# Performance work log

Measured on AMD Instinct MI355X. Metric: run time of the kernel, lower is better.

## Reference

```python
import jax, jax.numpy as jnp
import numpy as np

D, H1, O, E = 1024, 4096, 1024, 8
B = 8192


def setup_inputs() -> dict:
    key = jax.random.key(0)
    k1, k2, k3, k4 = jax.random.split(key, 4)
    # kaiming_uniform_ with nonlinearity='relu': bound = sqrt(6 / fan_in), fan_in = last dim
    b_w1 = float(np.sqrt(6.0 / D))
    b_w2 = float(np.sqrt(6.0 / H1))
    x = jax.random.normal(k1, (B, D), dtype=jnp.float32)
    eid = jax.random.randint(k2, (B,), 0, E, dtype=jnp.int32)
    W1 = jax.random.uniform(k3, (E, H1, D), dtype=jnp.float32, minval=-b_w1, maxval=b_w1)
    W2 = jax.random.uniform(k4, (E, O, H1), dtype=jnp.float32, minval=-b_w2, maxval=b_w2)
    b2 = jnp.zeros((E, O), dtype=jnp.float32)
    return {"x": x, "eid": eid, "W1": W1, "W2": W2, "b2": b2}


def reference(x, eid, W1, W2, b2):
    # Per-token expert MLP: y_i = gelu(x_i @ W1[eid_i].T) @ W2[eid_i].T + b2[eid_i]
    # Dense-dispatch formulation: loop over the (small, static) expert axis,
    # compute each expert MLP on all tokens, and select per-token via mask.
    # Math is identical to the sort/gather/scatter original.
    y = jnp.zeros((x.shape[0], W2.shape[1]), dtype=x.dtype)
    for e in range(W1.shape[0]):
        h = jax.nn.gelu(x @ W1[e].T, approximate=False)   # [B, H1]
        y_e = h @ W2[e].T + b2[e]                          # [B, O]
        mask = (eid == e)[:, None].astype(x.dtype)
        y = y + mask * y_e
    return y
```

## Files before the change

### kernel.cpp

```cpp
#include <hip/hip_runtime.h>
#include <hip/hip_bf16.h>
#include <math.h>

constexpr int kD  = 1024;
constexpr int kH1 = 4096;
constexpr int kO  = 1024;
constexpr int kE  = 8;
constexpr int kB  = 8192;

constexpr int BM   = 128;
constexpr int MAXT = kB / BM + kE;

typedef __attribute__((ext_vector_type(8))) short short8;
typedef __attribute__((ext_vector_type(4))) float f32x4;

__device__ __forceinline__ unsigned short f2bf(float f) {
  unsigned int u = __float_as_uint(f);
  u += 0x7fffu + ((u >> 16) & 1u);
  return (unsigned short)(u >> 16);
}

__device__ __forceinline__ float gelu_fast(float x) {
  float u = 0.7978845608028654f * (x + 0.044715f * x * x * x);
  float eu = __expf(2.0f * u);
  float th = 1.0f - 2.0f / (eu + 1.0f);
  return 0.5f * x * (1.0f + th);
}

__device__ __forceinline__ void cvt8(const float* __restrict__ src,
                                     unsigned short* __restrict__ dst) {
  const float4* s = (const float4*)src;
  float4 f0 = s[0], f1 = s[1];
  short8 v;
  v[0] = (short)f2bf(f0.x); v[1] = (short)f2bf(f0.y);
  v[2] = (short)f2bf(f0.z); v[3] = (short)f2bf(f0.w);
  v[4] = (short)f2bf(f1.x); v[5] = (short)f2bf(f1.y);
  v[6] = (short)f2bf(f1.z); v[7] = (short)f2bf(f1.w);
  *(short8*)dst = v;
}

__global__ __launch_bounds__(256) void setup_kernel(const int* __restrict__ eid,
                                                    int* __restrict__ perm,
                                                    int* __restrict__ tiles) {
  __shared__ int cnt[kE];
  __shared__ int off[kE];
  __shared__ int cur[kE];
  int t = threadIdx.x;
  if (t < kE) { cnt[t] = 0; cur[t] = 0; }
  __syncthreads();
  for (int i = t; i < kB; i += 256) atomicAdd(&cnt[eid[i]], 1);
  __syncthreads();
  if (t == 0) {
    int o = 0, nt = 0;
    for (int e = 0; e < kE; ++e) {
      off[e] = o;
      int c = cnt[e];
      for (int r = 0; r < c; r += BM) {
        tiles[nt * 4 + 0] = e;
        tiles[nt * 4 + 1] = o + r;
        tiles[nt * 4 + 2] = (c - r < BM) ? (c - r) : BM;
        tiles[nt * 4 + 3] = 0;
        ++nt;
      }
      o += c;
    }
    for (; nt < MAXT; ++nt) {
      tiles[nt * 4 + 0] = 0; tiles[nt * 4 + 1] = 0;
      tiles[nt * 4 + 2] = 0; tiles[nt * 4 + 3] = 0;
    }
  }
  __syncthreads();
  for (int i = t; i < kB; i += 256) {
    int e = eid[i];
    int p = off[e] + atomicAdd(&cur[e], 1);
    perm[p] = i;
  }
}

constexpr int kGB = kB * kD / 8 / 256;
constexpr int kCN = kE * kH1 * kD / 8;

__global__ __launch_bounds__(256) void prep_kernel(
    const float* __restrict__ x, const int* __restrict__ perm,
    unsigned short* __restrict__ xg,
    const float* __restrict__ W1, unsigned short* __restrict__ W1b) {
  const int b = blockIdx.x;
  if (b < kGB) {
    int idx = b * 256 + threadIdx.x;
    int pos = idx >> 7;
    int c   = (idx & 127) << 3;
    cvt8(x + (size_t)perm[pos] * kD + c, xg + (size_t)pos * kD + c);
  } else {
    const int cb = b - kGB;
    const int stride = 2048 * 256;
    for (int i = cb * 256 + threadIdx.x; i < kCN; i += stride)
      cvt8(W1 + (size_t)i * 8, W1b + (size_t)i * 8);
  }
}

__global__ __launch_bounds__(256) void convert_kernel(const float* __restrict__ src,
                                                      unsigned short* __restrict__ dst,
                                                      int n8) {
  int stride = gridDim.x * 256;
  for (int i = blockIdx.x * 256 + threadIdx.x; i < n8; i += stride)
    cvt8(src + (size_t)i * 8, dst + (size_t)i * 8);
}

template <int KTOT, int N, int NPAN, int MODE, int CONVW2>
__global__ __launch_bounds__(512, 2) void gemm32_kernel(
    const unsigned short* __restrict__ Amat,
    const unsigned short* __restrict__ Bmat,
    const float* __restrict__ bias,
    const int* __restrict__ tiles,
    const int* __restrict__ perm,
    unsigned short* __restrict__ out_bf,
    float* __restrict__ out_f,
    const float* __restrict__ csrc,
    unsigned short* __restrict__ cdst) {
  extern __shared__ char lds[];
  constexpr int NKt = KTOT / 32;
  constexpr int TOTAL = MAXT * NPAN;
  constexpr int cpx = TOTAL / 8;
  constexpr int nchN = (NPAN >= 4) ? NPAN / 4 : 1;

  int bid = blockIdx.x;
  const int t = threadIdx.x;

  if constexpr (CONVW2 > 0) {
    if (bid < 256) {
      constexpr int per = kCN / 256;
      size_t u0 = (size_t)bid * per;
      for (int i = t; i < per; i += 512)
        cvt8(csrc + (u0 + i) * 8, cdst + (u0 + i) * 8);
      return;
    }
    bid -= 256;
  }

  const int id = (bid & 7) * cpx + (bid >> 3);
  const int chunk = id >> 4, a16 = id & 15;
  const int ti = (chunk / nchN) * 4 + (a16 & 3);
  const int n0 = ((chunk % nchN) * 4 + (a16 >> 2)) * 256;

  const int e  = tiles[ti * 4 + 0];
  const int rs = tiles[ti * 4 + 1];
  const int nr = tiles[ti * 4 + 2];
  if (nr == 0) return;

  const int l = t & 63;
  const int w = t >> 6;
  const int lr = l & 15, g = l >> 4;
  const int wr = w >> 2;
  const int wc = w & 3;

  const unsigned short* Bp = Bmat + (size_t)e * N * KTOT;

  const int sR = t >> 2;
  const int sG = (t & 3) ^ ((sR >> 1) & 3);
  const unsigned short* ArowS = Amat + (size_t)(rs + sR) * KTOT + sG * 8;
  const unsigned short* BrowS0 = Bp + (size_t)(n0 + sR) * KTOT + sG * 8;
  const unsigned short* BrowS1 = Bp + (size_t)(n0 + 128 + sR) * KTOT + sG * 8;

  auto stageA = [&](char* buf, int k0) {
    __builtin_amdgcn_global_load_lds(
        (const __attribute__((address_space(1))) unsigned int*)(ArowS + k0),
        (__attribute__((address_space(3))) unsigned int*)(buf + t * 16), 16, 0, 0);
  };
  auto stageB = [&](char* buf, int k0, int i) {
    const unsigned short* src = (i ? BrowS1 : BrowS0) + k0;
    __builtin_amdgcn_global_load_lds(
        (const __attribute__((address_space(1))) unsigned int*)src,
        (__attribute__((address_space(3))) unsigned int*)(buf + 8192 + i * 8192 + t * 16),
        16, 0, 0);
  };

  const int rA = wr * 64 + lr;
  const int rB = wc * 64 + lr;
  const int offA0 = rA * 64 + ((g ^ ((rA >> 1) & 3)) * 16);
  const int offB0 = 8192 + rB * 64 + ((g ^ ((rB >> 1) & 3)) * 16);

  short8 aF[4], bF[4];
  f32x4 acc[4][4] = {};

  auto readA = [&](char* buf) {
#pragma unroll
    for (int mr = 0; mr < 4; ++mr)
      aF[mr] = *(const short8*)(buf + offA0 + mr * 1024);
  };
  auto readB2 = [&](char* buf, int nclo) {
#pragma unroll
    for (int j = 0; j < 2; ++j)
      bF[nclo + j] = *(const short8*)(buf + offB0 + (nclo + j) * 1024);
  };
  auto mfmaH = [&](int nclo) {
    __builtin_amdgcn_s_setprio(1);
#pragma unroll
    for (int j = 0; j < 2; ++j)
#pragma unroll
      for (int mr = 0; mr < 4; ++mr)
        acc[nclo + j][mr] = __builtin_amdgcn_mfma_f32_16x16x32_bf16(
            aF[mr], bF[nclo + j], acc[nclo + j][mr], 0, 0, 0);
    __builtin_amdgcn_s_setprio(0);
  };

  char* b0 = lds;
  char* b1 = lds + 24576;
  char* b2 = lds + 49152;

  stageA(b0, 0);  stageB(b0, 0, 0);  stageB(b0, 0, 1);
  stageA(b1, 32); stageB(b1, 32, 0); stageB(b1, 32, 1);

#pragma unroll 1
  for (int kt = 0; kt < NKt; ++kt) {
    const int k0n = (kt + 2) * 32;
    const bool more = (kt + 2 < NKt);
    if (kt == NKt - 1) asm volatile("s_waitcnt vmcnt(0)" ::: "memory");
    else               asm volatile("s_waitcnt vmcnt(3)" ::: "memory");
    __builtin_amdgcn_s_barrier();
    readA(b0);
    readB2(b0, 0);
    if (more) stageA(b2, k0n);
    __builtin_amdgcn_s_barrier();
    mfmaH(0);
    __builtin_amdgcn_s_barrier();
    readB2(b0, 2);
    if (more) { stageB(b2, k0n, 0); stageB(b2, k0n, 1); }
    __builtin_amdgcn_s_barrier();
    mfmaH(2);
    char* tmp = b0; b0 = b1; b1 = b2; b2 = tmp;
  }

  const int lr4 = g * 4;
#pragma unroll
  for (int mr = 0; mr < 4; ++mr)
#pragma unroll
    for (int rg = 0; rg < 4; ++rg) {
      int row = wr * 64 + mr * 16 + lr4 + rg;
      if (row < nr) {
        if constexpr (MODE == 0) {
          unsigned short* dst = out_bf + (size_t)(rs + row) * N + n0 + wc * 64;
#pragma unroll
          for (int nc = 0; nc < 4; ++nc)
            dst[nc * 16 + lr] = f2bf(gelu_fast(acc[nc][mr][rg]));
        } else {
          int orig = perm[rs + row];
          float* dst = out_f + (size_t)orig * N + n0 + wc * 64;
          const float* bp = bias + (size_t)e * N + n0 + wc * 64;
#pragma unroll
          for (int nc = 0; nc < 4; ++nc)
            dst[nc * 16 + lr] = acc[nc][mr][rg] + bp[nc * 16 + lr];
        }
      }
    }
}

extern "C" void kernel_launch(void* const* d_in, const int* in_sizes, int n_in,
                              void* d_out, int out_size, void* d_ws, size_t ws_size,
                              hipStream_t stream) {
  const float* x  = (const float*)d_in[0];
  const int*  eid = (const int*)d_in[1];
  const float* W1 = (const float*)d_in[2];
  const float* W2 = (const float*)d_in[3];
  const float* b2 = (const float*)d_in[4];
  float* y = (float*)d_out;

  char* ws = (char*)d_ws;
  int* perm  = (int*)ws;
  int* tiles = (int*)(ws + 32768);
  unsigned short* xg = (unsigned short*)(ws + 36864);
  size_t xg_bytes = (size_t)(kB + 128) * kD * 2;
  unsigned short* h  = (unsigned short*)(ws + 36864 + xg_bytes);
  size_t h_bytes = (size_t)(kB + 128) * kH1 * 2;
  size_t w1b_off = 36864 + xg_bytes + h_bytes;
  unsigned short* W1b = (unsigned short*)(ws + w1b_off);
  size_t w2b_off = w1b_off + 67108864;
  const bool twobuf = ws_size >= w2b_off + 67108864;
  unsigned short* W2b = twobuf ? (unsigned short*)(ws + w2b_off) : W1b;

  auto g1f = gemm32_kernel<kD, kH1, 16, 0, 1>;
  auto g1s = gemm32_kernel<kD, kH1, 16, 0, 0>;
  auto g2  = gemm32_kernel<kH1, kO, 4, 1, 0>;
  hipFuncSetAttribute((const void*)g1f, hipFuncAttributeMaxDynamicSharedMemorySize, 73728);
  hipFuncSetAttribute((const void*)g1s, hipFuncAttributeMaxDynamicSharedMemorySize, 73728);
  hipFuncSetAttribute((const void*)g2,  hipFuncAttributeMaxDynamicSharedMemorySize, 73728);

  setup_kernel<<<1, 256, 0, stream>>>(eid, perm, tiles);

  prep_kernel<<<kGB + 2048, 256, 0, stream>>>(x, perm, xg, W1, W1b);

  if (twobuf) {
    g1f<<<256 + MAXT * 16, 512, 73728, stream>>>(
        xg, W1b, nullptr, tiles, perm, h, nullptr, W2, W2b);
  } else {
    g1s<<<MAXT * 16, 512, 73728, stream>>>(
        xg, W1b, nullptr, tiles, perm, h, nullptr, nullptr, nullptr);
    convert_kernel<<<2048, 256, 0, stream>>>(W2, W2b, kCN);
  }

  g2<<<MAXT * 4, 512, 73728, stream>>>(
      h, W2b, b2, tiles, perm, nullptr, y, nullptr, nullptr);
}
```

Before: 303.2 us.

## Split-K the second expert GEMM in two halves with a bf16 partial and a reduce pass

The second GEMM's K dimension (4096) is split into two halves, so the grid doubles from MAXT*4 to MAXT*8 blocks and the device is better filled. The first half writes fp32 results straight to y. The second half writes a bf16 partial into the reused xg buffer. A new reduce kernel adds that partial plus the bias into y. This trades an extra kernel launch, extra memory traffic and bf16 rounding of half the partial sum for more parallelism in a GEMM that previously had too few blocks.

```diff
diff --git a/kernel.cpp b/kernel.cpp
--- a/kernel.cpp
+++ b/kernel.cpp
@@ -18,6 +18,9 @@
   unsigned int u = __float_as_uint(f);
   u += 0x7fffu + ((u >> 16) & 1u);
   return (unsigned short)(u >> 16);
+}
+__device__ __forceinline__ float bf2f(unsigned short u) {
+  return __uint_as_float(((unsigned int)u) << 16);
 }
 
 __device__ __forceinline__ float gelu_fast(float x) {
@@ -118,7 +121,7 @@
     const float* __restrict__ csrc,
     unsigned short* __restrict__ cdst) {
   extern __shared__ char lds[];
-  constexpr int NKt = KTOT / 32;
+  constexpr int NKt = (MODE == 1) ? (KTOT / 64) : (KTOT / 32);
   constexpr int TOTAL = MAXT * NPAN;
   constexpr int cpx = TOTAL / 8;
   constexpr int nchN = (NPAN >= 4) ? NPAN / 4 : 1;
@@ -140,7 +143,14 @@
   const int id = (bid & 7) * cpx + (bid >> 3);
   const int chunk = id >> 4, a16 = id & 15;
   const int ti = (chunk / nchN) * 4 + (a16 & 3);
-  const int n0 = ((chunk % nchN) * 4 + (a16 >> 2)) * 256;
+  const int pancol = (chunk % nchN) * 4 + (a16 >> 2);
+
+  int n0, kb, half;
+  if constexpr (MODE == 0) {
+    n0 = pancol * 256; kb = 0; half = 0;
+  } else {
+    half = pancol >> 2; n0 = (pancol & 3) * 256; kb = half * (KTOT / 2);
+  }
 
   const int e  = tiles[ti * 4 + 0];
   const int rs = tiles[ti * 4 + 1];
@@ -157,9 +167,9 @@
 
   const int sR = t >> 2;
   const int sG = (t & 3) ^ ((sR >> 1) & 3);
-  const unsigned short* ArowS = Amat + (size_t)(rs + sR) * KTOT + sG * 8;
-  const unsigned short* BrowS0 = Bp + (size_t)(n0 + sR) * KTOT + sG * 8;
-  const unsigned short* BrowS1 = Bp + (size_t)(n0 + 128 + sR) * KTOT + sG * 8;
+  const unsigned short* ArowS = Amat + (size_t)(rs + sR) * KTOT + kb + sG * 8;
+  const unsigned short* BrowS0 = Bp + (size_t)(n0 + sR) * KTOT + kb + sG * 8;
+  const unsigned short* BrowS1 = Bp + (size_t)(n0 + 128 + sR) * KTOT + kb + sG * 8;
 
   auto stageA = [&](char* buf, int k0) {
     __builtin_amdgcn_global_load_lds(
@@ -243,15 +253,47 @@
           for (int nc = 0; nc < 4; ++nc)
             dst[nc * 16 + lr] = f2bf(gelu_fast(acc[nc][mr][rg]));
         } else {
-          int orig = perm[rs + row];
-          float* dst = out_f + (size_t)orig * N + n0 + wc * 64;
-          const float* bp = bias + (size_t)e * N + n0 + wc * 64;
-#pragma unroll
-          for (int nc = 0; nc < 4; ++nc)
-            dst[nc * 16 + lr] = acc[nc][mr][rg] + bp[nc * 16 + lr];
+          if (half == 0) {
+            float* dst = out_f + (size_t)perm[rs + row] * N + n0 + wc * 64;
+#pragma unroll
+            for (int nc = 0; nc < 4; ++nc)
+              dst[nc * 16 + lr] = acc[nc][mr][rg];
+          } else {
+            unsigned short* dst = out_bf + (size_t)(rs + row) * N + n0 + wc * 64;
+#pragma unroll
+            for (int nc = 0; nc < 4; ++nc)
+              dst[nc * 16 + lr] = f2bf(acc[nc][mr][rg]);
+          }
         }
       }
     }
+}
+
+__global__ __launch_bounds__(256) void reduce_kernel(float* __restrict__ y,
+                                                     const unsigned short* __restrict__ part,
+                                                     const int* __restrict__ perm,
+                                                     const int* __restrict__ eid,
+                                                     const float* __restrict__ b2) {
+  int idx = blockIdx.x * 256 + threadIdx.x;
+  int p = idx >> 7;
+  int c = (idx & 127) << 3;
+  int orig = perm[p];
+  int e = eid[orig];
+  float* yp = y + (size_t)orig * kO + c;
+  short8 pv = *(const short8*)(part + (size_t)p * kO + c);
+  const float* bp = b2 + (size_t)e * kO + c;
+  float4 y0 = *(float4*)yp, y1 = *(float4*)(yp + 4);
+  float4 b0 = *(const float4*)bp, b1 = *(const float4*)(bp + 4);
+  y0.x += bf2f((unsigned short)pv[0]) + b0.x;
+  y0.y += bf2f((unsigned short)pv[1]) + b0.y;
+  y0.z += bf2f((unsigned short)pv[2]) + b0.z;
+  y0.w += bf2f((unsigned short)pv[3]) + b0.w;
+  y1.x += bf2f((unsigned short)pv[4]) + b1.x;
+  y1.y += bf2f((unsigned short)pv[5]) + b1.y;
+  y1.z += bf2f((unsigned short)pv[6]) + b1.z;
+  y1.w += bf2f((unsigned short)pv[7]) + b1.w;
+  *(float4*)yp = y0;
+  *(float4*)(yp + 4) = y1;
 }
 
 extern "C" void kernel_launch(void* const* d_in, const int* in_sizes, int n_in,
@@ -279,10 +321,10 @@
 
   auto g1f = gemm32_kernel<kD, kH1, 16, 0, 1>;
   auto g1s = gemm32_kernel<kD, kH1, 16, 0, 0>;
-  auto g2  = gemm32_kernel<kH1, kO, 4, 1, 0>;
-  hipFuncSetAttribute((const void*)g1f, hipFuncAttributeMaxDynamicSharedMemorySize, 73728);
-  hipFuncSetAttribute((const void*)g1s, hipFuncAttributeMaxDynamicSharedMemorySize, 73728);
-  hipFuncSetAttribute((const void*)g2,  hipFuncAttributeMaxDynamicSharedMemorySize, 73728);
+  auto g2  = gemm32_kernel<kH1, kO, 8, 1, 0>;
+  (void)hipFuncSetAttribute((const void*)g1f, hipFuncAttributeMaxDynamicSharedMemorySize, 73728);
+  (void)hipFuncSetAttribute((const void*)g1s, hipFuncAttributeMaxDynamicSharedMemorySize, 73728);
+  (void)hipFuncSetAttribute((const void*)g2,  hipFuncAttributeMaxDynamicSharedMemorySize, 73728);
 
   setup_kernel<<<1, 256, 0, stream>>>(eid, perm, tiles);
 
@@ -297,6 +339,8 @@
     convert_kernel<<<2048, 256, 0, stream>>>(W2, W2b, kCN);
   }
 
-  g2<<<MAXT * 4, 512, 73728, stream>>>(
-      h, W2b, b2, tiles, perm, nullptr, y, nullptr, nullptr);
-}
+  g2<<<MAXT * 8, 512, 73728, stream>>>(
+      h, W2b, b2, tiles, perm, xg, y, nullptr, nullptr);
+
+  reduce_kernel<<<(kB * kO / 8) / 256, 256, 0, stream>>>(y, xg, perm, eid, b2);
+}
```

After: 311.6 us. +2.8%, slower.

## Load A fragments directly from global memory and shrink LDS to raise occupancy

Applied to the files above, without the earlier changes.

Removes LDS staging of the activation operand: each wave now loads its A fragments straight from global memory every k-step, while only the weight tiles use the three-buffer LDS pipeline. This cuts LDS usage and barriers per iteration so four blocks per CU fit, and the second GEMM uses narrower 128-column tiles with more blocks. The W2 bf16 conversion is no longer fused into the first GEMM and runs as a separate kernel. The risk is exposed global-load latency for A, which is not prefetched, and redundant A traffic across column blocks.

```diff
diff --git a/kernel.cpp b/kernel.cpp
--- a/kernel.cpp
+++ b/kernel.cpp
@@ -106,47 +106,37 @@
     cvt8(src + (size_t)i * 8, dst + (size_t)i * 8);
 }
 
-template <int KTOT, int N, int NPAN, int MODE, int CONVW2>
-__global__ __launch_bounds__(512, 2) void gemm32_kernel(
+template <int KTOT, int N, int NPAN, int BN, int MODE>
+__global__ __launch_bounds__(512, 4) void gemmad_kernel(
     const unsigned short* __restrict__ Amat,
     const unsigned short* __restrict__ Bmat,
     const float* __restrict__ bias,
     const int* __restrict__ tiles,
     const int* __restrict__ perm,
     unsigned short* __restrict__ out_bf,
-    float* __restrict__ out_f,
-    const float* __restrict__ csrc,
-    unsigned short* __restrict__ cdst) {
+    float* __restrict__ out_f) {
   extern __shared__ char lds[];
-  constexpr int NKt = KTOT / 32;
+  constexpr int NKt  = KTOT / 32;
+  constexpr int BISS = BN / 128;
+  constexpr int NC   = BN / 64;
+  constexpr int BUFB = BN * 64;
   constexpr int TOTAL = MAXT * NPAN;
   constexpr int cpx = TOTAL / 8;
   constexpr int nchN = (NPAN >= 4) ? NPAN / 4 : 1;
 
-  int bid = blockIdx.x;
-  const int t = threadIdx.x;
-
-  if constexpr (CONVW2 > 0) {
-    if (bid < 256) {
-      constexpr int per = kCN / 256;
-      size_t u0 = (size_t)bid * per;
-      for (int i = t; i < per; i += 512)
-        cvt8(csrc + (u0 + i) * 8, cdst + (u0 + i) * 8);
-      return;
-    }
-    bid -= 256;
-  }
-
+  const int bid = blockIdx.x;
   const int id = (bid & 7) * cpx + (bid >> 3);
   const int chunk = id >> 4, a16 = id & 15;
   const int ti = (chunk / nchN) * 4 + (a16 & 3);
-  const int n0 = ((chunk % nchN) * 4 + (a16 >> 2)) * 256;
+  const int pancol = (chunk % nchN) * 4 + (a16 >> 2);
+  const int n0 = pancol * BN;
 
   const int e  = tiles[ti * 4 + 0];
   const int rs = tiles[ti * 4 + 1];
   const int nr = tiles[ti * 4 + 2];
   if (nr == 0) return;
 
+  const int t = threadIdx.x;
   const int l = t & 63;
   const int w = t >> 6;
   const int lr = l & 15, g = l >> 4;
@@ -155,78 +145,66 @@
 
   const unsigned short* Bp = Bmat + (size_t)e * N * KTOT;
 
+  const unsigned short* A0 = Amat + (size_t)(rs + wr * 64 + 0 * 16 + lr) * KTOT + g * 8;
+  const unsigned short* A1 = Amat + (size_t)(rs + wr * 64 + 1 * 16 + lr) * KTOT + g * 8;
+  const unsigned short* A2 = Amat + (size_t)(rs + wr * 64 + 2 * 16 + lr) * KTOT + g * 8;
+  const unsigned short* A3 = Amat + (size_t)(rs + wr * 64 + 3 * 16 + lr) * KTOT + g * 8;
+
   const int sR = t >> 2;
   const int sG = (t & 3) ^ ((sR >> 1) & 3);
-  const unsigned short* ArowS = Amat + (size_t)(rs + sR) * KTOT + sG * 8;
   const unsigned short* BrowS0 = Bp + (size_t)(n0 + sR) * KTOT + sG * 8;
   const unsigned short* BrowS1 = Bp + (size_t)(n0 + 128 + sR) * KTOT + sG * 8;
 
-  auto stageA = [&](char* buf, int k0) {
+  auto stageB = [&](char* buf, int k0) {
     __builtin_amdgcn_global_load_lds(
-        (const __attribute__((address_space(1))) unsigned int*)(ArowS + k0),
+        (const __attribute__((address_space(1))) unsigned int*)(BrowS0 + k0),
         (__attribute__((address_space(3))) unsigned int*)(buf + t * 16), 16, 0, 0);
+    if constexpr (BISS == 2)
+      __builtin_amdgcn_global_load_lds(
+          (const __attribute__((address_space(1))) unsigned int*)(BrowS1 + k0),
+          (__attribute__((address_space(3))) unsigned int*)(buf + 8192 + t * 16),
+          16, 0, 0);
   };
-  auto stageB = [&](char* buf, int k0, int i) {
-    const unsigned short* src = (i ? BrowS1 : BrowS0) + k0;
-    __builtin_amdgcn_global_load_lds(
-        (const __attribute__((address_space(1))) unsigned int*)src,
-        (__attribute__((address_space(3))) unsigned int*)(buf + 8192 + i * 8192 + t * 16),
-        16, 0, 0);
-  };
-
-  const int rA = wr * 64 + lr;
-  const int rB = wc * 64 + lr;
-  const int offA0 = rA * 64 + ((g ^ ((rA >> 1) & 3)) * 16);
-  const int offB0 = 8192 + rB * 64 + ((g ^ ((rB >> 1) & 3)) * 16);
-
-  short8 aF[4], bF[4];
-  f32x4 acc[4][4] = {};
-
-  auto readA = [&](char* buf) {
-#pragma unroll
-    for (int mr = 0; mr < 4; ++mr)
-      aF[mr] = *(const short8*)(buf + offA0 + mr * 1024);
-  };
-  auto readB2 = [&](char* buf, int nclo) {
-#pragma unroll
-    for (int j = 0; j < 2; ++j)
-      bF[nclo + j] = *(const short8*)(buf + offB0 + (nclo + j) * 1024);
-  };
-  auto mfmaH = [&](int nclo) {
+
+  const int rB0 = wc * (BN / 4) + lr;
+  const int offB0 = rB0 * 64 + ((g ^ ((rB0 >> 1) & 3)) * 16);
+
+  short8 aF[4], bF[NC];
+  f32x4 acc[NC][4] = {};
+
+  auto mfmaAll = [&]() {
     __builtin_amdgcn_s_setprio(1);
 #pragma unroll
-    for (int j = 0; j < 2; ++j)
+    for (int nc = 0; nc < NC; ++nc)
 #pragma unroll
       for (int mr = 0; mr < 4; ++mr)
-        acc[nclo + j][mr] = __builtin_amdgcn_mfma_f32_16x16x32_bf16(
-            aF[mr], bF[nclo + j], acc[nclo + j][mr], 0, 0, 0);
+        acc[nc][mr] = __builtin_amdgcn_mfma_f32_16x16x32_bf16(
+            aF[mr], bF[nc], acc[nc][mr], 0, 0, 0);
     __builtin_amdgcn_s_setprio(0);
   };
 
   char* b0 = lds;
-  char* b1 = lds + 24576;
-  char* b2 = lds + 49152;
-
-  stageA(b0, 0);  stageB(b0, 0, 0);  stageB(b0, 0, 1);
-  stageA(b1, 32); stageB(b1, 32, 0); stageB(b1, 32, 1);
+  char* b1 = lds + BUFB;
+  char* b2 = lds + 2 * BUFB;
+
+  stageB(b0, 0);
+  stageB(b1, 32);
 
 #pragma unroll 1
   for (int kt = 0; kt < NKt; ++kt) {
-    const int k0n = (kt + 2) * 32;
-    const bool more = (kt + 2 < NKt);
-    if (kt == NKt - 1) asm volatile("s_waitcnt vmcnt(0)" ::: "memory");
-    else               asm volatile("s_waitcnt vmcnt(3)" ::: "memory");
+    if constexpr (BISS == 2) asm volatile("s_waitcnt vmcnt(2)" ::: "memory");
+    else                     asm volatile("s_waitcnt vmcnt(1)" ::: "memory");
     __builtin_amdgcn_s_barrier();
-    readA(b0);
-    readB2(b0, 0);
-    if (more) stageA(b2, k0n);
-    __builtin_amdgcn_s_barrier();
-    mfmaH(0);
-    __builtin_amdgcn_s_barrier();
-    readB2(b0, 2);
-    if (more) { stageB(b2, k0n, 0); stageB(b2, k0n, 1); }
-    __builtin_amdgcn_s_barrier();
-    mfmaH(2);
+    const int k0 = kt * 32;
+    aF[0] = *(const short8*)(A0 + k0);
+    aF[1] = *(const short8*)(A1 + k0);
+    aF[2] = *(const short8*)(A2 + k0);
+    aF[3] = *(const short8*)(A3 + k0);
+#pragma unroll
+    for (int nc = 0; nc < NC; ++nc)
+      bF[nc] = *(const short8*)(b0 + offB0 + nc * 1024);
+    if (kt + 2 < NKt) stageB(b2, (kt + 2) * 32);
+    mfmaAll();
     char* tmp = b0; b0 = b1; b1 = b2; b2 = tmp;
   }
 
@@ -238,16 +216,16 @@
       int row = wr * 64 + mr * 16 + lr4 + rg;
       if (row < nr) {
         if constexpr (MODE == 0) {
-          unsigned short* dst = out_bf + (size_t)(rs + row) * N + n0 + wc * 64;
-#pragma unroll
-          for (int nc = 0; nc < 4; ++nc)
+          unsigned short* dst = out_bf + (size_t)(rs + row) * N + n0 + wc * (BN / 4);
+#pragma unroll
+          for (int nc = 0; nc < NC; ++nc)
             dst[nc * 16 + lr] = f2bf(gelu_fast(acc[nc][mr][rg]));
         } else {
           int orig = perm[rs + row];
-          float* dst = out_f + (size_t)orig * N + n0 + wc * 64;
-          const float* bp = bias + (size_t)e * N + n0 + wc * 64;
-#pragma unroll
-          for (int nc = 0; nc < 4; ++nc)
+          float* dst = out_f + (size_t)orig * N + n0 + wc * (BN / 4);
+          const float* bp = bias + (size_t)e * N + n0 + wc * (BN / 4);
+#pragma unroll
+          for (int nc = 0; nc < NC; ++nc)
             dst[nc * 16 + lr] = acc[nc][mr][rg] + bp[nc * 16 + lr];
         }
       }
@@ -277,26 +255,18 @@
   const bool twobuf = ws_size >= w2b_off + 67108864;
   unsigned short* W2b = twobuf ? (unsigned short*)(ws + w2b_off) : W1b;
 
-  auto g1f = gemm32_kernel<kD, kH1, 16, 0, 1>;
-  auto g1s = gemm32_kernel<kD, kH1, 16, 0, 0>;
-  auto g2  = gemm32_kernel<kH1, kO, 4, 1, 0>;
-  hipFuncSetAttribute((const void*)g1f, hipFuncAttributeMaxDynamicSharedMemorySize, 73728);
-  hipFuncSetAttribute((const void*)g1s, hipFuncAttributeMaxDynamicSharedMemorySize, 73728);
-  hipFuncSetAttribute((const void*)g2,  hipFuncAttributeMaxDynamicSharedMemorySize, 73728);
+  auto g1 = gemmad_kernel<kD, kH1, 16, 256, 0>;
+  auto g2 = gemmad_kernel<kH1, kO, 8, 128, 1>;
+  (void)hipFuncSetAttribute((const void*)g1, hipFuncAttributeMaxDynamicSharedMemorySize, 49152);
+  (void)hipFuncSetAttribute((const void*)g2, hipFuncAttributeMaxDynamicSharedMemorySize, 24576);
 
   setup_kernel<<<1, 256, 0, stream>>>(eid, perm, tiles);
 
   prep_kernel<<<kGB + 2048, 256, 0, stream>>>(x, perm, xg, W1, W1b);
 
-  if (twobuf) {
-    g1f<<<256 + MAXT * 16, 512, 73728, stream>>>(
-        xg, W1b, nullptr, tiles, perm, h, nullptr, W2, W2b);
-  } else {
-    g1s<<<MAXT * 16, 512, 73728, stream>>>(
-        xg, W1b, nullptr, tiles, perm, h, nullptr, nullptr, nullptr);
-    convert_kernel<<<2048, 256, 0, stream>>>(W2, W2b, kCN);
-  }
-
-  g2<<<MAXT * 4, 512, 73728, stream>>>(
-      h, W2b, b2, tiles, perm, nullptr, y, nullptr, nullptr);
-}
+  g1<<<MAXT * 16, 512, 49152, stream>>>(xg, W1b, nullptr, tiles, perm, h, nullptr);
+
+  convert_kernel<<<2048, 256, 0, stream>>>(W2, W2b, kCN);
+
+  g2<<<MAXT * 8, 512, 24576, stream>>>(h, W2b, b2, tiles, perm, nullptr, y);
+}
```

Result: slower. 676.8 us (+123.2%).
